# Kernel tuning notes

Hardware: AMD Instinct MI355X
Metric: run time of the kernel (lower is better)

The kernel has to match this reference:

```python
import jax, jax.numpy as jnp
import numpy as np

N_CHARS = 50257
CHAR = 512
HID = 1024
LENGTH = 2048


def setup_inputs() -> dict:
    key = jax.random.key(0)
    ks = jax.random.split(key, 8)
    s = 1.0 / np.sqrt(HID)
    sh = 1.0 / np.sqrt(HID)
    return {
        "inputs": jax.random.normal(ks[0], (HID,), jnp.float32),
        "embed": (jax.random.normal(ks[1], (N_CHARS, CHAR), jnp.float32) * 0.02),
        "W_ih": jax.random.uniform(ks[2], (4 * HID, CHAR), jnp.float32, -s, s),
        "W_hh": jax.random.uniform(ks[3], (4 * HID, HID), jnp.float32, -s, s),
        "b_ih": jax.random.uniform(ks[4], (4 * HID,), jnp.float32, -s, s),
        "b_hh": jax.random.uniform(ks[5], (4 * HID,), jnp.float32, -s, s),
        "W_head": jax.random.uniform(ks[6], (N_CHARS, HID), jnp.float32, -sh, sh),
        "b_head": jax.random.uniform(ks[7], (N_CHARS,), jnp.float32, -sh, sh),
        "length": LENGTH,
        "start": 5,
    }


def _lstm_cell(x, h, c, W_ih, W_hh, b_ih, b_hh):
    # PyTorch gate order: i, f, g, o
    gates = W_ih @ x + b_ih + W_hh @ h + b_hh  # [4H]
    i, f, g, o = jnp.split(gates, 4)
    i = jax.nn.sigmoid(i)
    f = jax.nn.sigmoid(f)
    g = jnp.tanh(g)
    o = jax.nn.sigmoid(o)
    c = f * c + i * g
    h = o * jnp.tanh(c)
    return h, c


def reference(inputs, embed, W_ih, W_hh, b_ih, b_hh, W_head, b_head, length, start):
    h0 = inputs                       # latent used as initial hidden state
    c0 = jnp.zeros_like(inputs)
    x0 = embed[start]                 # [CHAR]

    def step(carry, _):
        h, c, x = carry
        h, c = _lstm_cell(x, h, c, W_ih, W_hh, b_ih, b_hh)
        logits = W_head @ h + b_head  # [N_CHARS]
        char = jnp.argmax(logits)
        x = embed[char]
        return (h, c, x), (char, logits)

    _, (chars, logits) = jax.lax.scan(step, (h0, c0, x0), None, length=length)
    return chars, logits
```

## Files before the change

kernel.cpp:

```cpp
#include <hip/hip_runtime.h>
#include <stdint.h>
#include <math.h>

#define HID   1024
#define CHARD 512
#define NC    50257
#define TLEN  2048
#define NBS   1571
#define NBH   1571
#define SQ    4064.0f
#define INVSQ (1.0f/4064.0f)
#define QERR  (0.5f/4064.0f)
#define CANDR 256

typedef unsigned long long ull;
typedef unsigned char u8;
typedef float f32x4 __attribute__((ext_vector_type(4)));

__device__ __forceinline__ unsigned ford(float f) {
    unsigned b = __float_as_uint(f);
    return (b & 0x80000000u) ? ~b : (b | 0x80000000u);
}
__device__ __forceinline__ float unford(unsigned u) {
    return __uint_as_float((u & 0x80000000u) ? (u & 0x7FFFFFFFu) : ~u);
}
__device__ __forceinline__ ull packkv(float v, unsigned j) {
    return ((ull)ford(v) << 32) | (ull)(0xFFFFFFFFu - j);
}
__device__ __forceinline__ ull umaxu(ull a, ull b) { return a > b ? a : b; }
__device__ __forceinline__ ull shflx_ull(ull v, int m) {
    unsigned lo = (unsigned)v, hi = (unsigned)(v >> 32);
    lo = __shfl_xor(lo, m);
    hi = __shfl_xor(hi, m);
    return ((ull)hi << 32) | lo;
}

__global__ __launch_bounds__(256) void k_init(const float* __restrict__ inputs,
                                              float* __restrict__ hh,
                                              float* __restrict__ c)
{
    int tid = blockIdx.x * 256 + threadIdx.x;
    if (tid < HID) { hh[tid] = inputs[tid]; c[tid] = 0.f; }
}

__global__ __launch_bounds__(256) void k_quant(const float* __restrict__ W,
                                               u8* __restrict__ W8)
{
    size_t base = ((size_t)blockIdx.x * 256 + threadIdx.x) * 16;
    if (base >= (size_t)NC * HID) return;
    const float4* src = (const float4*)(W + base);
    uint out[4];
    #pragma unroll
    for (int g = 0; g < 4; ++g) {
        float4 w = src[g];
        int a0 = __float2int_rn(w.x * SQ) & 255;
        int a1 = __float2int_rn(w.y * SQ) & 255;
        int a2 = __float2int_rn(w.z * SQ) & 255;
        int a3 = __float2int_rn(w.w * SQ) & 255;
        out[g] = (uint)(a0 | (a1 << 8) | (a2 << 16) | (a3 << 24));
    }
    *(uint4*)(W8 + base) = make_uint4(out[0], out[1], out[2], out[3]);
}

__device__ __forceinline__ float exact_logit(const float4* hs4,
                                             const float* __restrict__ W_head,
                                             const float* __restrict__ b_head,
                                             int j, int lane)
{
    const float4* wr = (const float4*)(W_head + (size_t)j * HID);
    float a = 0.f;
    #pragma unroll
    for (int m = 0; m < 4; ++m) {
        float4 w = wr[m * 64 + lane], v = hs4[m * 64 + lane];
        a = fmaf(w.x, v.x, a); a = fmaf(w.y, v.y, a);
        a = fmaf(w.z, v.z, a); a = fmaf(w.w, v.w, a);
    }
    #pragma unroll
    for (int off = 32; off > 0; off >>= 1) a += __shfl_xor(a, off);
    return a + b_head[j];
}

__device__ __forceinline__ unsigned resolve_char(const float4* hs4,
                                                 const ull* __restrict__ blockmax,
                                                 const float* __restrict__ abuf,
                                                 const float* __restrict__ W_head,
                                                 const float* __restrict__ b_head,
                                                 float Sh, ull* red4, int tid)
{
    __shared__ int s_cnt;
    __shared__ int s_rows[CANDR];

    const int wave = tid >> 6;
    const int lane = tid & 63;

    ull pm = 0ull;
    for (int i = tid; i < NBS; i += 256) pm = umaxu(pm, blockmax[i]);
    #pragma unroll
    for (int off = 32; off > 0; off >>= 1) pm = umaxu(pm, shflx_ull(pm, off));
    if (lane == 0) red4[wave] = pm;
    if (tid == 0) s_cnt = 0;
    __syncthreads();
    pm = umaxu(umaxu(red4[0], red4[1]), umaxu(red4[2], red4[3]));
    const float mtil = unford((unsigned)(pm >> 32));
    const float E = QERR * Sh * 1.02f + 1e-4f;
    const float thresh = mtil - 2.0f * E;
    const ull pkth = ((ull)ford(thresh)) << 32;
    __syncthreads();

    for (int i = tid; i < NBS; i += 256) {
        if (blockmax[i] >= pkth) {
            const int jbase = i * 32;
            #pragma unroll
            for (int r = 0; r < 32; ++r) {
                const int j = jbase + r;
                if (j < NC && abuf[j] >= thresh) {
                    int p = atomicAdd(&s_cnt, 1);
                    if (p < CANDR) s_rows[p] = j;
                }
            }
        }
    }
    __syncthreads();
    const int ncr = s_cnt;

    ull best = 0ull;
    if (ncr <= CANDR) {
        for (int q = wave; q < ncr; q += 4) {
            const int j = s_rows[q];
            const float v = exact_logit(hs4, W_head, b_head, j, lane);
            best = umaxu(best, packkv(v, (unsigned)j));
        }
    } else {
        for (int i = wave; i < NBS; i += 4) {
            if (blockmax[i] >= pkth) {
                const int jbase = i * 32;
                for (int rr = 0; rr < 32; ++rr) {
                    const int j = jbase + rr;
                    if (j >= NC) break;
                    if (abuf[j] >= thresh) {
                        const float v = exact_logit(hs4, W_head, b_head, j, lane);
                        best = umaxu(best, packkv(v, (unsigned)j));
                    }
                }
            }
        }
    }
    __syncthreads();
    if (lane == 0) red4[wave] = best;
    __syncthreads();
    best = umaxu(umaxu(red4[0], red4[1]), umaxu(red4[2], red4[3]));
    unsigned idx = 0xFFFFFFFFu - (unsigned)(best & 0xFFFFFFFFull);
    return idx < NC ? idx : (NC - 1);
}

__global__ __launch_bounds__(256) void k_lstm(const float* __restrict__ W_ih,
                                              const float* __restrict__ W_hh,
                                              const float* __restrict__ b_ih,
                                              const float* __restrict__ b_hh,
                                              const float* __restrict__ embed,
                                              const float* __restrict__ W_head,
                                              const float* __restrict__ b_head,
                                              const ull* __restrict__ blockmax,
                                              const float* __restrict__ abuf,
                                              const float* __restrict__ h_in,
                                              float* __restrict__ h_out,
                                              float* __restrict__ c,
                                              float* __restrict__ chars_out,
                                              const int* __restrict__ startp,
                                              int t)
{
    __shared__ float4 xs4[CHARD / 4];
    __shared__ float4 hs4[HID / 4];
    __shared__ ull    red4[4];
    __shared__ float  sred[4];

    const int tid  = threadIdx.x;
    const int wave = tid >> 6;
    const int lane = tid & 63;

    float4 hv = ((const float4*)h_in)[tid];
    hs4[tid] = hv;
    float sa = fabsf(hv.x) + fabsf(hv.y) + fabsf(hv.z) + fabsf(hv.w);
    #pragma unroll
    for (int off = 32; off > 0; off >>= 1) sa += __shfl_xor(sa, off);
    if (lane == 0) sred[wave] = sa;
    __syncthreads();
    const float Sh = sred[0] + sred[1] + sred[2] + sred[3];

    unsigned idx;
    if (t == 0) {
        idx = (unsigned)startp[0];
    } else {
        idx = resolve_char(hs4, blockmax, abuf, W_head, b_head, Sh, red4, tid);
        if (blockIdx.x == 0 && tid == 0) chars_out[t - 1] = (float)idx;
    }

    const float4* ex = (const float4*)(embed + (size_t)idx * CHARD);
    if (tid < 128) xs4[tid] = ex[tid];
    __syncthreads();

    const int r = blockIdx.x * 4 + wave;

    float acc[4];
    #pragma unroll
    for (int q = 0; q < 4; ++q) {
        const float4* wi = (const float4*)(W_ih + (size_t)(q * HID + r) * CHARD);
        const float4* wh = (const float4*)(W_hh + (size_t)(q * HID + r) * HID);
        float a = 0.f;
        #pragma unroll
        for (int m = 0; m < 2; ++m) {
            float4 w = wi[m * 64 + lane], v = xs4[m * 64 + lane];
            a = fmaf(w.x, v.x, a); a = fmaf(w.y, v.y, a);
            a = fmaf(w.z, v.z, a); a = fmaf(w.w, v.w, a);
        }
        #pragma unroll
        for (int m = 0; m < 4; ++m) {
            float4 w = wh[m * 64 + lane], v = hs4[m * 64 + lane];
            a = fmaf(w.x, v.x, a); a = fmaf(w.y, v.y, a);
            a = fmaf(w.z, v.z, a); a = fmaf(w.w, v.w, a);
        }
        acc[q] = a;
    }
    #pragma unroll
    for (int q = 0; q < 4; ++q) {
        #pragma unroll
        for (int off = 32; off > 0; off >>= 1) acc[q] += __shfl_xor(acc[q], off);
    }

    if (lane == 0) {
        float zi = acc[0] + b_ih[r]           + b_hh[r];
        float zf = acc[1] + b_ih[HID + r]     + b_hh[HID + r];
        float zg = acc[2] + b_ih[2 * HID + r] + b_hh[2 * HID + r];
        float zo = acc[3] + b_ih[3 * HID + r] + b_hh[3 * HID + r];
        float ig = 1.f / (1.f + expf(-zi));
        float fg = 1.f / (1.f + expf(-zf));
        float gg = tanhf(zg);
        float og = 1.f / (1.f + expf(-zo));
        float cn = fg * c[r] + ig * gg;
        c[r] = cn;
        h_out[r] = og * tanhf(cn);
    }
}

__global__ __launch_bounds__(256) void k_screen(const u8* __restrict__ W8,
                                                const float* __restrict__ b_head,
                                                const float* __restrict__ h_in,
                                                float* __restrict__ abuf,
                                                ull* __restrict__ blockmax)
{
    __shared__ float4 hs4[HID / 4];
    __shared__ ull    wred[4];

    const int tid  = threadIdx.x;
    const int wave = tid >> 6;
    const int lane = tid & 63;

    hs4[tid] = ((const float4*)h_in)[tid];
    __syncthreads();

    const float4 h0 = hs4[lane * 4 + 0];
    const float4 h1 = hs4[lane * 4 + 1];
    const float4 h2 = hs4[lane * 4 + 2];
    const float4 h3 = hs4[lane * 4 + 3];

    const int base = blockIdx.x * 32 + wave * 8;
    ull pm = 0ull;
    #pragma unroll
    for (int rep = 0; rep < 8; ++rep) {
        const int j = base + rep;
        if (j < NC) {
            uint4 q = ((const uint4*)(W8 + (size_t)j * HID))[lane];
            float a = 0.f;
            a = fmaf((float)((int)(q.x << 24) >> 24), h0.x, a);
            a = fmaf((float)((int)(q.x << 16) >> 24), h0.y, a);
            a = fmaf((float)((int)(q.x <<  8) >> 24), h0.z, a);
            a = fmaf((float)((int)(q.x      ) >> 24), h0.w, a);
            a = fmaf((float)((int)(q.y << 24) >> 24), h1.x, a);
            a = fmaf((float)((int)(q.y << 16) >> 24), h1.y, a);
            a = fmaf((float)((int)(q.y <<  8) >> 24), h1.z, a);
            a = fmaf((float)((int)(q.y      ) >> 24), h1.w, a);
            a = fmaf((float)((int)(q.z << 24) >> 24), h2.x, a);
            a = fmaf((float)((int)(q.z << 16) >> 24), h2.y, a);
            a = fmaf((float)((int)(q.z <<  8) >> 24), h2.z, a);
            a = fmaf((float)((int)(q.z      ) >> 24), h2.w, a);
            a = fmaf((float)((int)(q.w << 24) >> 24), h3.x, a);
            a = fmaf((float)((int)(q.w << 16) >> 24), h3.y, a);
            a = fmaf((float)((int)(q.w <<  8) >> 24), h3.z, a);
            a = fmaf((float)((int)(q.w      ) >> 24), h3.w, a);
            #pragma unroll
            for (int off = 32; off > 0; off >>= 1) a += __shfl_xor(a, off);
            const float v = a * INVSQ + b_head[j];
            if (lane == 0) abuf[j] = v;
            pm = umaxu(pm, packkv(v, (unsigned)j));
        }
    }
    if (lane == 0) wred[wave] = pm;
    __syncthreads();
    if (tid == 0)
        blockmax[blockIdx.x] = umaxu(umaxu(wred[0], wred[1]), umaxu(wred[2], wred[3]));
}

__global__ __launch_bounds__(256) void k_finalc(const float* __restrict__ h_in,
                                                const ull* __restrict__ blockmax,
                                                const float* __restrict__ abuf,
                                                const float* __restrict__ W_head,
                                                const float* __restrict__ b_head,
                                                float* __restrict__ chars_out)
{
    __shared__ float4 hs4[HID / 4];
    __shared__ ull    red4[4];
    __shared__ float  sred[4];
    const int tid  = threadIdx.x;
    const int wave = tid >> 6;
    const int lane = tid & 63;

    float4 hv = ((const float4*)h_in)[tid];
    hs4[tid] = hv;
    float sa = fabsf(hv.x) + fabsf(hv.y) + fabsf(hv.z) + fabsf(hv.w);
    #pragma unroll
    for (int off = 32; off > 0; off >>= 1) sa += __shfl_xor(sa, off);
    if (lane == 0) sred[wave] = sa;
    __syncthreads();
    const float Sh = sred[0] + sred[1] + sred[2] + sred[3];
    unsigned idx = resolve_char(hs4, blockmax, abuf, W_head, b_head, Sh, red4, tid);
    if (tid == 0) chars_out[TLEN - 1] = (float)idx;
}

#define GJ 64
#define GT 128
#define GK 16
__global__ __launch_bounds__(256) void k_gemm(const float* __restrict__ W_head,
                                              const float* __restrict__ b_head,
                                              const float* __restrict__ hh,
                                              float* __restrict__ logits)
{
    __shared__ float Ws[GK][GJ + 4];
    __shared__ float Hs[GK][GT + 1];

    const int tid = threadIdx.x;
    const int j0 = blockIdx.x * GJ;
    const int t0 = blockIdx.y * GT;
    const int tj = tid & 15;
    const int tt = tid >> 4;

    const int wlj = tid >> 2;
    const int wlk = (tid & 3) * 4;
    const int hlt = tid >> 1;
    const int hlk = (tid & 1) * 8;
    const float* Wrow = W_head + (size_t)(j0 + wlj) * HID;
    const bool wvalid = (j0 + wlj) < NC;

    float acc[8][4];
    #pragma unroll
    for (int b = 0; b < 8; ++b)
        #pragma unroll
        for (int a = 0; a < 4; ++a) acc[b][a] = 0.f;

    for (int k0 = 0; k0 < HID; k0 += GK) {
        __syncthreads();
        float4 wv = wvalid ? *(const float4*)(Wrow + k0 + wlk) : make_float4(0, 0, 0, 0);
        Ws[wlk + 0][wlj] = wv.x; Ws[wlk + 1][wlj] = wv.y;
        Ws[wlk + 2][wlj] = wv.z; Ws[wlk + 3][wlj] = wv.w;
        const float* hp = hh + (size_t)(t0 + hlt + 1) * HID + k0 + hlk;
        float4 a0 = *(const float4*)hp;
        float4 a1 = *(const float4*)(hp + 4);
        Hs[hlk + 0][hlt] = a0.x; Hs[hlk + 1][hlt] = a0.y;
        Hs[hlk + 2][hlt] = a0.z; Hs[hlk + 3][hlt] = a0.w;
        Hs[hlk + 4][hlt] = a1.x; Hs[hlk + 5][hlt] = a1.y;
        Hs[hlk + 6][hlt] = a1.z; Hs[hlk + 7][hlt] = a1.w;
        __syncthreads();
        #pragma unroll
        for (int kk = 0; kk < GK; ++kk) {
            float4 w4 = *(const float4*)&Ws[kk][tj * 4];
            float hvv[8];
            #pragma unroll
            for (int b = 0; b < 8; ++b) hvv[b] = Hs[kk][tt + 16 * b];
            #pragma unroll
            for (int b = 0; b < 8; ++b) {
                acc[b][0] = fmaf(w4.x, hvv[b], acc[b][0]);
                acc[b][1] = fmaf(w4.y, hvv[b], acc[b][1]);
                acc[b][2] = fmaf(w4.z, hvv[b], acc[b][2]);
                acc[b][3] = fmaf(w4.w, hvv[b], acc[b][3]);
            }
        }
    }

    const int j = j0 + tj * 4;
    float b0 = (j + 0 < NC) ? b_head[j + 0] : 0.f;
    float b1 = (j + 1 < NC) ? b_head[j + 1] : 0.f;
    float b2 = (j + 2 < NC) ? b_head[j + 2] : 0.f;
    float b3 = (j + 3 < NC) ? b_head[j + 3] : 0.f;
    #pragma unroll
    for (int b = 0; b < 8; ++b) {
        const int t = t0 + tt + 16 * b;
        float* dst = logits + (size_t)t * NC + j;
        if (j + 3 < NC) {
            f32x4 o = { acc[b][0] + b0, acc[b][1] + b1,
                        acc[b][2] + b2, acc[b][3] + b3 };
            __builtin_nontemporal_store(o, (f32x4*)dst);
        } else {
            if (j + 0 < NC) dst[0] = acc[b][0] + b0;
            if (j + 1 < NC) dst[1] = acc[b][1] + b1;
            if (j + 2 < NC) dst[2] = acc[b][2] + b2;
        }
    }
}

__global__ __launch_bounds__(256) void k_init_fb(const float* __restrict__ inputs,
                                                 const int* __restrict__ startp,
                                                 float* __restrict__ h0,
                                                 float* __restrict__ c,
                                                 ull* __restrict__ blockmax)
{
    int tid = blockIdx.x * 256 + threadIdx.x;
    if (tid < NBH) blockmax[tid] = (tid == 0) ? packkv(3.0e38f, (unsigned)startp[0]) : 0ull;
    if (tid < HID) { h0[tid] = inputs[tid]; c[tid] = 0.f; }
}

__global__ __launch_bounds__(256) void k_lstm_fb(const float* __restrict__ W_ih,
                                                 const float* __restrict__ W_hh,
                                                 const float* __restrict__ b_ih,
                                                 const float* __restrict__ b_hh,
                                                 const float* __restrict__ embed,
                                                 const ull* __restrict__ blockmax,
                                                 const float* __restrict__ h_in,
                                                 float* __restrict__ h_out,
                                                 float* __restrict__ c,
                                                 float* __restrict__ chars_out,
                                                 int t)
{
    __shared__ float4 xs4[CHARD / 4];
    __shared__ float4 hs4[HID / 4];
    __shared__ ull    red[256];
    const int tid = threadIdx.x;
    ull pm = 0ull;
    for (int i = tid; i < NBH; i += 256) pm = umaxu(pm, blockmax[i]);
    red[tid] = pm;
    __syncthreads();
    for (int s = 128; s > 0; s >>= 1) {
        if (tid < s) red[tid] = umaxu(red[tid], red[tid + s]);
        __syncthreads();
    }
    const unsigned idx = 0xFFFFFFFFu - (unsigned)(red[0] & 0xFFFFFFFFull);
    if (t > 0 && blockIdx.x == 0 && tid == 0) chars_out[t - 1] = (float)idx;
    const float4* ex = (const float4*)(embed + (size_t)idx * CHARD);
    if (tid < 128) xs4[tid] = ex[tid];
    hs4[tid] = ((const float4*)h_in)[tid];
    __syncthreads();
    const int wave = tid >> 6, lane = tid & 63;
    const int r = blockIdx.x * 4 + wave;
    float acc[4];
    #pragma unroll
    for (int q = 0; q < 4; ++q) {
        const float4* wi = (const float4*)(W_ih + (size_t)(q * HID + r) * CHARD);
        const float4* wh = (const float4*)(W_hh + (size_t)(q * HID + r) * HID);
        float a = 0.f;
        #pragma unroll
        for (int m = 0; m < 2; ++m) {
            float4 w = wi[m * 64 + lane], v = xs4[m * 64 + lane];
            a = fmaf(w.x, v.x, a); a = fmaf(w.y, v.y, a);
            a = fmaf(w.z, v.z, a); a = fmaf(w.w, v.w, a);
        }
        #pragma unroll
        for (int m = 0; m < 4; ++m) {
            float4 w = wh[m * 64 + lane], v = hs4[m * 64 + lane];
            a = fmaf(w.x, v.x, a); a = fmaf(w.y, v.y, a);
            a = fmaf(w.z, v.z, a); a = fmaf(w.w, v.w, a);
        }
        acc[q] = a;
    }
    #pragma unroll
    for (int q = 0; q < 4; ++q)
        #pragma unroll
        for (int off = 32; off > 0; off >>= 1) acc[q] += __shfl_xor(acc[q], off);
    if (lane == 0) {
        float zi = acc[0] + b_ih[r]           + b_hh[r];
        float zf = acc[1] + b_ih[HID + r]     + b_hh[HID + r];
        float zg = acc[2] + b_ih[2 * HID + r] + b_hh[2 * HID + r];
        float zo = acc[3] + b_ih[3 * HID + r] + b_hh[3 * HID + r];
        float ig = 1.f / (1.f + expf(-zi));
        float fg = 1.f / (1.f + expf(-zf));
        float gg = tanhf(zg);
        float og = 1.f / (1.f + expf(-zo));
        float cn = fg * c[r] + ig * gg;
        c[r] = cn;
        h_out[r] = og * tanhf(cn);
    }
}

__global__ __launch_bounds__(256) void k_head_fb(const float* __restrict__ W_head,
                                                 const float* __restrict__ b_head,
                                                 const float* __restrict__ h_in,
                                                 float* __restrict__ logits,
                                                 ull* __restrict__ blockmax)
{
    __shared__ float4 hs4[HID / 4];
    __shared__ ull    wmax[4];
    const int tid = threadIdx.x;
    hs4[tid] = ((const float4*)h_in)[tid];
    __syncthreads();
    const int wave = tid >> 6, lane = tid & 63;
    const int base = blockIdx.x * 32 + wave * 8;
    ull pm = 0ull;
    #pragma unroll
    for (int rep = 0; rep < 8; ++rep) {
        const int j = base + rep;
        if (j < NC) {
            const float4* w = (const float4*)(W_head + (size_t)j * HID);
            float a = 0.f;
            #pragma unroll
            for (int m = 0; m < 4; ++m) {
                float4 ww = w[m * 64 + lane], v = hs4[m * 64 + lane];
                a = fmaf(ww.x, v.x, a); a = fmaf(ww.y, v.y, a);
                a = fmaf(ww.z, v.z, a); a = fmaf(ww.w, v.w, a);
            }
            #pragma unroll
            for (int off = 32; off > 0; off >>= 1) a += __shfl_xor(a, off);
            const float v = a + b_head[j];
            if (lane == 0) __builtin_nontemporal_store(v, &logits[j]);
            pm = umaxu(pm, packkv(v, (unsigned)j));
        }
    }
    if (lane == 0) wmax[wave] = pm;
    __syncthreads();
    if (tid == 0)
        blockmax[blockIdx.x] = umaxu(umaxu(wmax[0], wmax[1]), umaxu(wmax[2], wmax[3]));
}

__global__ __launch_bounds__(256) void k_final_fb(const ull* __restrict__ blockmax,
                                                  float* __restrict__ chars_out)
{
    __shared__ ull red[256];
    const int tid = threadIdx.x;
    ull pm = 0ull;
    for (int i = tid; i < NBH; i += 256) pm = umaxu(pm, blockmax[i]);
    red[tid] = pm;
    __syncthreads();
    for (int s = 128; s > 0; s >>= 1) {
        if (tid < s) red[tid] = umaxu(red[tid], red[tid + s]);
        __syncthreads();
    }
    if (tid == 0)
        chars_out[TLEN - 1] = (float)(0xFFFFFFFFu - (unsigned)(red[0] & 0xFFFFFFFFull));
}

extern "C" void kernel_launch(void* const* d_in, const int* in_sizes, int n_in,
                              void* d_out, int out_size, void* d_ws, size_t ws_size,
                              hipStream_t stream)
{
    const float* inputs = (const float*)d_in[0];
    const float* embed  = (const float*)d_in[1];
    const float* W_ih   = (const float*)d_in[2];
    const float* W_hh   = (const float*)d_in[3];
    const float* b_ih   = (const float*)d_in[4];
    const float* b_hh   = (const float*)d_in[5];
    const float* W_head = (const float*)d_in[6];
    const float* b_head = (const float*)d_in[7];
    const int*   startp = (const int*)d_in[9];

    float* out        = (float*)d_out;
    float* chars_out  = out;
    float* logits_out = out + TLEN;

    char* ws = (char*)d_ws;
    const size_t off_hh = 0;
    const size_t off_c  = off_hh + (size_t)(TLEN + 1) * HID * 4;
    const size_t off_ab = off_c + (size_t)HID * 4;
    const size_t off_bm = (off_ab + (size_t)NC * 4 + 7) & ~(size_t)7;
    const size_t off_w8 = (off_bm + (size_t)NBS * 8 + 15) & ~(size_t)15;
    const size_t need   = off_w8 + (size_t)NC * HID;

    if (ws_size >= need) {
        float* hh   = (float*)(ws + off_hh);
        float* c    = (float*)(ws + off_c);
        float* abuf = (float*)(ws + off_ab);
        ull*   bm   = (ull*)(ws + off_bm);
        u8*    W8   = (u8*)(ws + off_w8);

        hipLaunchKernelGGL(k_init, dim3(4), dim3(256), 0, stream, inputs, hh, c);
        hipLaunchKernelGGL(k_quant, dim3((NC * HID / 16 + 255) / 256), dim3(256), 0, stream,
                           W_head, W8);

        for (int t = 0; t < TLEN; ++t) {
            hipLaunchKernelGGL(k_lstm, dim3(256), dim3(256), 0, stream,
                               W_ih, W_hh, b_ih, b_hh, embed, W_head, b_head,
                               bm, abuf, hh + (size_t)t * HID, hh + (size_t)(t + 1) * HID,
                               c, chars_out, startp, t);
            hipLaunchKernelGGL(k_screen, dim3(NBS), dim3(256), 0, stream,
                               W8, b_head, hh + (size_t)(t + 1) * HID, abuf, bm);
        }
        hipLaunchKernelGGL(k_finalc, dim3(1), dim3(256), 0, stream,
                           hh + (size_t)TLEN * HID, bm, abuf, W_head, b_head, chars_out);
        hipLaunchKernelGGL(k_gemm, dim3((NC + GJ - 1) / GJ, TLEN / GT), dim3(256), 0, stream,
                           W_head, b_head, hh, logits_out);
    } else {
        float* h0 = (float*)(ws);
        float* h1 = (float*)(ws + 4096);
        float* c  = (float*)(ws + 8192);
        ull* blockmax = (ull*)(ws + 12288);
        hipLaunchKernelGGL(k_init_fb, dim3(7), dim3(256), 0, stream,
                           inputs, startp, h0, c, blockmax);
        for (int t = 0; t < TLEN; ++t) {
            const float* hin = (t & 1) ? h1 : h0;
            float*       hout = (t & 1) ? h0 : h1;
            hipLaunchKernelGGL(k_lstm_fb, dim3(256), dim3(256), 0, stream,
                               W_ih, W_hh, b_ih, b_hh, embed, blockmax,
                               hin, hout, c, chars_out, t);
            hipLaunchKernelGGL(k_head_fb, dim3(NBH), dim3(256), 0, stream,
                               W_head, b_head, hout,
                               logits_out + (size_t)t * NC, blockmax);
        }
        hipLaunchKernelGGL(k_final_fb, dim3(1), dim3(256), 0, stream, blockmax, chars_out);
    }
}
```

Before: 54.27 ms.

## Fuse per-step LSTM and screen kernels into one persistent kernel with grid barriers

Replaces the 4096 per-step kernel launches (LSTM cell plus int8 head screening) with a single persistent 256-block kernel that loops over all timesteps, using a custom flag-based grid barrier between phases. Each block caches its W_ih/W_hh rows in shared memory and keeps the cell state in a register. The head screening is re-partitioned into 1024 groups of 50 rows, one per wave. This removes launch overhead and repeated weight reloads. In exchange it relies on all 256 blocks being co-resident, and the spin barrier carries a deadlock/timeout risk and its own synchronisation cost.

```diff
diff --git a/kernel.cpp b/kernel.cpp
--- a/kernel.cpp
+++ b/kernel.cpp
@@ -6,12 +6,15 @@
 #define CHARD 512
 #define NC    50257
 #define TLEN  2048
-#define NBS   1571
+#define NBLK  256
+#define NGRP2 1024
+#define GR    50
 #define NBH   1571
 #define SQ    4064.0f
 #define INVSQ (1.0f/4064.0f)
 #define QERR  (0.5f/4064.0f)
 #define CANDR 256
+#define FLAGSTRIDE 16
 
 typedef unsigned long long ull;
 typedef unsigned char u8;
@@ -35,12 +38,48 @@
     return ((ull)hi << 32) | lo;
 }
 
+__device__ __forceinline__ void gridbar(unsigned* flags, unsigned* gen,
+                                        unsigned k, int b, int tid)
+{
+    __syncthreads();
+    if (b == 0) {
+        if (tid == 0) {
+            __threadfence();
+            __hip_atomic_store(&flags[0], k, __ATOMIC_RELAXED, __HIP_MEMORY_SCOPE_AGENT);
+        }
+        unsigned v; int guard = 0;
+        do {
+            v = __hip_atomic_load(&flags[tid * FLAGSTRIDE], __ATOMIC_RELAXED,
+                                  __HIP_MEMORY_SCOPE_AGENT);
+        } while (v < k && ++guard < (1 << 27));
+        __syncthreads();
+        if (tid == 0)
+            __hip_atomic_store(gen, k, __ATOMIC_RELAXED, __HIP_MEMORY_SCOPE_AGENT);
+    } else {
+        if (tid == 0) {
+            __threadfence();
+            __hip_atomic_store(&flags[b * FLAGSTRIDE], k, __ATOMIC_RELAXED,
+                               __HIP_MEMORY_SCOPE_AGENT);
+            unsigned v; int guard = 0;
+            do {
+                __builtin_amdgcn_s_sleep(1);
+                v = __hip_atomic_load(gen, __ATOMIC_RELAXED, __HIP_MEMORY_SCOPE_AGENT);
+            } while (v < k && ++guard < (1 << 27));
+        }
+        __syncthreads();
+    }
+    if (tid == 0) __threadfence();
+    __syncthreads();
+}
+
 __global__ __launch_bounds__(256) void k_init(const float* __restrict__ inputs,
                                               float* __restrict__ hh,
-                                              float* __restrict__ c)
-{
-    int tid = blockIdx.x * 256 + threadIdx.x;
-    if (tid < HID) { hh[tid] = inputs[tid]; c[tid] = 0.f; }
+                                              float* __restrict__ c,
+                                              unsigned* __restrict__ flagarea)
+{
+    int g = blockIdx.x * 256 + threadIdx.x;
+    if (g < HID) { hh[g] = inputs[g]; c[g] = 0.f; }
+    for (int i = g; i < NBLK * FLAGSTRIDE + 16; i += 2048) flagarea[i] = 0u;
 }
 
 __global__ __launch_bounds__(256) void k_quant(const float* __restrict__ W,
@@ -81,7 +120,7 @@
 }
 
 __device__ __forceinline__ unsigned resolve_char(const float4* hs4,
-                                                 const ull* __restrict__ blockmax,
+                                                 const ull* __restrict__ bm,
                                                  const float* __restrict__ abuf,
                                                  const float* __restrict__ W_head,
                                                  const float* __restrict__ b_head,
@@ -94,7 +133,9 @@
     const int lane = tid & 63;
 
     ull pm = 0ull;
-    for (int i = tid; i < NBS; i += 256) pm = umaxu(pm, blockmax[i]);
+    #pragma unroll
+    for (int rep = 0; rep < NGRP2 / 256; ++rep)
+        pm = umaxu(pm, bm[tid + rep * 256]);
     #pragma unroll
     for (int off = 32; off > 0; off >>= 1) pm = umaxu(pm, shflx_ull(pm, off));
     if (lane == 0) red4[wave] = pm;
@@ -107,13 +148,14 @@
     const ull pkth = ((ull)ford(thresh)) << 32;
     __syncthreads();
 
-    for (int i = tid; i < NBS; i += 256) {
-        if (blockmax[i] >= pkth) {
-            const int jbase = i * 32;
-            #pragma unroll
-            for (int r = 0; r < 32; ++r) {
-                const int j = jbase + r;
-                if (j < NC && abuf[j] >= thresh) {
+    #pragma unroll
+    for (int rep = 0; rep < NGRP2 / 256; ++rep) {
+        const int i = tid + rep * 256;
+        if (bm[i] >= pkth) {
+            const int jb = i * GR;
+            const int je = jb + GR < NC ? jb + GR : NC;
+            for (int j = jb; j < je; ++j) {
+                if (abuf[j] >= thresh) {
                     int p = atomicAdd(&s_cnt, 1);
                     if (p < CANDR) s_rows[p] = j;
                 }
@@ -127,20 +169,18 @@
     if (ncr <= CANDR) {
         for (int q = wave; q < ncr; q += 4) {
             const int j = s_rows[q];
-            const float v = exact_logit(hs4, W_head, b_head, j, lane);
-            best = umaxu(best, packkv(v, (unsigned)j));
+            best = umaxu(best, packkv(exact_logit(hs4, W_head, b_head, j, lane),
+                                      (unsigned)j));
         }
     } else {
-        for (int i = wave; i < NBS; i += 4) {
-            if (blockmax[i] >= pkth) {
-                const int jbase = i * 32;
-                for (int rr = 0; rr < 32; ++rr) {
-                    const int j = jbase + rr;
-                    if (j >= NC) break;
-                    if (abuf[j] >= thresh) {
-                        const float v = exact_logit(hs4, W_head, b_head, j, lane);
-                        best = umaxu(best, packkv(v, (unsigned)j));
-                    }
+        for (int i = wave; i < NGRP2; i += 4) {
+            if (bm[i] >= pkth) {
+                const int jb = i * GR;
+                const int je = jb + GR < NC ? jb + GR : NC;
+                for (int j = jb; j < je; ++j) {
+                    if (abuf[j] >= thresh)
+                        best = umaxu(best, packkv(exact_logit(hs4, W_head, b_head, j, lane),
+                                                  (unsigned)j));
                 }
             }
         }
@@ -153,177 +193,157 @@
     return idx < NC ? idx : (NC - 1);
 }
 
-__global__ __launch_bounds__(256) void k_lstm(const float* __restrict__ W_ih,
-                                              const float* __restrict__ W_hh,
-                                              const float* __restrict__ b_ih,
-                                              const float* __restrict__ b_hh,
-                                              const float* __restrict__ embed,
-                                              const float* __restrict__ W_head,
-                                              const float* __restrict__ b_head,
-                                              const ull* __restrict__ blockmax,
-                                              const float* __restrict__ abuf,
-                                              const float* __restrict__ h_in,
-                                              float* __restrict__ h_out,
-                                              float* __restrict__ c,
-                                              float* __restrict__ chars_out,
-                                              const int* __restrict__ startp,
-                                              int t)
-{
+__global__ __launch_bounds__(256) void k_persist(
+    const float* __restrict__ W_ih, const float* __restrict__ W_hh,
+    const float* __restrict__ b_ih, const float* __restrict__ b_hh,
+    const float* __restrict__ embed,
+    const float* __restrict__ W_head, const float* __restrict__ b_head,
+    const u8* __restrict__ W8,
+    float* __restrict__ hh, float* __restrict__ abuf, ull* __restrict__ bm,
+    float* __restrict__ chars_out, const int* __restrict__ startp,
+    unsigned* flags, unsigned* gen)
+{
+    __shared__ float4 wiL[4][4][128];
+    __shared__ float4 whL[4][4][256];
     __shared__ float4 xs4[CHARD / 4];
     __shared__ float4 hs4[HID / 4];
     __shared__ ull    red4[4];
     __shared__ float  sred[4];
 
+    const int b    = blockIdx.x;
     const int tid  = threadIdx.x;
     const int wave = tid >> 6;
     const int lane = tid & 63;
-
-    float4 hv = ((const float4*)h_in)[tid];
-    hs4[tid] = hv;
-    float sa = fabsf(hv.x) + fabsf(hv.y) + fabsf(hv.z) + fabsf(hv.w);
-    #pragma unroll
-    for (int off = 32; off > 0; off >>= 1) sa += __shfl_xor(sa, off);
-    if (lane == 0) sred[wave] = sa;
-    __syncthreads();
-    const float Sh = sred[0] + sred[1] + sred[2] + sred[3];
-
-    unsigned idx;
-    if (t == 0) {
-        idx = (unsigned)startp[0];
-    } else {
-        idx = resolve_char(hs4, blockmax, abuf, W_head, b_head, Sh, red4, tid);
-        if (blockIdx.x == 0 && tid == 0) chars_out[t - 1] = (float)idx;
-    }
-
-    const float4* ex = (const float4*)(embed + (size_t)idx * CHARD);
-    if (tid < 128) xs4[tid] = ex[tid];
-    __syncthreads();
-
-    const int r = blockIdx.x * 4 + wave;
-
-    float acc[4];
-    #pragma unroll
+    const int r    = b * 4 + wave;
+
     for (int q = 0; q < 4; ++q) {
         const float4* wi = (const float4*)(W_ih + (size_t)(q * HID + r) * CHARD);
+        for (int m = lane; m < 128; m += 64) wiL[wave][q][m] = wi[m];
         const float4* wh = (const float4*)(W_hh + (size_t)(q * HID + r) * HID);
-        float a = 0.f;
-        #pragma unroll
-        for (int m = 0; m < 2; ++m) {
-            float4 w = wi[m * 64 + lane], v = xs4[m * 64 + lane];
-            a = fmaf(w.x, v.x, a); a = fmaf(w.y, v.y, a);
-            a = fmaf(w.z, v.z, a); a = fmaf(w.w, v.w, a);
-        }
-        #pragma unroll
-        for (int m = 0; m < 4; ++m) {
-            float4 w = wh[m * 64 + lane], v = hs4[m * 64 + lane];
-            a = fmaf(w.x, v.x, a); a = fmaf(w.y, v.y, a);
-            a = fmaf(w.z, v.z, a); a = fmaf(w.w, v.w, a);
-        }
-        acc[q] = a;
-    }
-    #pragma unroll
-    for (int q = 0; q < 4; ++q) {
-        #pragma unroll
-        for (int off = 32; off > 0; off >>= 1) acc[q] += __shfl_xor(acc[q], off);
-    }
-
-    if (lane == 0) {
-        float zi = acc[0] + b_ih[r]           + b_hh[r];
-        float zf = acc[1] + b_ih[HID + r]     + b_hh[HID + r];
-        float zg = acc[2] + b_ih[2 * HID + r] + b_hh[2 * HID + r];
-        float zo = acc[3] + b_ih[3 * HID + r] + b_hh[3 * HID + r];
-        float ig = 1.f / (1.f + expf(-zi));
-        float fg = 1.f / (1.f + expf(-zf));
-        float gg = tanhf(zg);
-        float og = 1.f / (1.f + expf(-zo));
-        float cn = fg * c[r] + ig * gg;
-        c[r] = cn;
-        h_out[r] = og * tanhf(cn);
-    }
-}
-
-__global__ __launch_bounds__(256) void k_screen(const u8* __restrict__ W8,
-                                                const float* __restrict__ b_head,
-                                                const float* __restrict__ h_in,
-                                                float* __restrict__ abuf,
-                                                ull* __restrict__ blockmax)
-{
-    __shared__ float4 hs4[HID / 4];
-    __shared__ ull    wred[4];
-
-    const int tid  = threadIdx.x;
-    const int wave = tid >> 6;
-    const int lane = tid & 63;
-
-    hs4[tid] = ((const float4*)h_in)[tid];
-    __syncthreads();
-
-    const float4 h0 = hs4[lane * 4 + 0];
-    const float4 h1 = hs4[lane * 4 + 1];
-    const float4 h2 = hs4[lane * 4 + 2];
-    const float4 h3 = hs4[lane * 4 + 3];
-
-    const int base = blockIdx.x * 32 + wave * 8;
-    ull pm = 0ull;
-    #pragma unroll
-    for (int rep = 0; rep < 8; ++rep) {
-        const int j = base + rep;
-        if (j < NC) {
-            uint4 q = ((const uint4*)(W8 + (size_t)j * HID))[lane];
+        for (int m = lane; m < 256; m += 64) whL[wave][q][m] = wh[m];
+    }
+    float bsum[4];
+    #pragma unroll
+    for (int q = 0; q < 4; ++q) bsum[q] = b_ih[q * HID + r] + b_hh[q * HID + r];
+    float creg = 0.f;
+    __syncthreads();
+
+    unsigned bk = 0;
+
+    for (int t = 0; t < TLEN; ++t) {
+        float4 hv = ((const float4*)(hh + (size_t)t * HID))[tid];
+        hs4[tid] = hv;
+        float sa = fabsf(hv.x) + fabsf(hv.y) + fabsf(hv.z) + fabsf(hv.w);
+        #pragma unroll
+        for (int off = 32; off > 0; off >>= 1) sa += __shfl_xor(sa, off);
+        if (lane == 0) sred[wave] = sa;
+        __syncthreads();
+        const float Sh = sred[0] + sred[1] + sred[2] + sred[3];
+
+        unsigned idx;
+        if (t == 0) {
+            idx = (unsigned)startp[0];
+        } else {
+            idx = resolve_char(hs4, bm, abuf, W_head, b_head, Sh, red4, tid);
+            if (b == 0 && tid == 0) chars_out[t - 1] = (float)idx;
+        }
+        if (tid < 128) xs4[tid] = ((const float4*)(embed + (size_t)idx * CHARD))[tid];
+        __syncthreads();
+
+        float acc[4];
+        #pragma unroll
+        for (int q = 0; q < 4; ++q) {
             float a = 0.f;
-            a = fmaf((float)((int)(q.x << 24) >> 24), h0.x, a);
-            a = fmaf((float)((int)(q.x << 16) >> 24), h0.y, a);
-            a = fmaf((float)((int)(q.x <<  8) >> 24), h0.z, a);
-            a = fmaf((float)((int)(q.x      ) >> 24), h0.w, a);
-            a = fmaf((float)((int)(q.y << 24) >> 24), h1.x, a);
-            a = fmaf((float)((int)(q.y << 16) >> 24), h1.y, a);
-            a = fmaf((float)((int)(q.y <<  8) >> 24), h1.z, a);
-            a = fmaf((float)((int)(q.y      ) >> 24), h1.w, a);
-            a = fmaf((float)((int)(q.z << 24) >> 24), h2.x, a);
-            a = fmaf((float)((int)(q.z << 16) >> 24), h2.y, a);
-            a = fmaf((float)((int)(q.z <<  8) >> 24), h2.z, a);
-            a = fmaf((float)((int)(q.z      ) >> 24), h2.w, a);
-            a = fmaf((float)((int)(q.w << 24) >> 24), h3.x, a);
-            a = fmaf((float)((int)(q.w << 16) >> 24), h3.y, a);
-            a = fmaf((float)((int)(q.w <<  8) >> 24), h3.z, a);
-            a = fmaf((float)((int)(q.w      ) >> 24), h3.w, a);
             #pragma unroll
-            for (int off = 32; off > 0; off >>= 1) a += __shfl_xor(a, off);
-            const float v = a * INVSQ + b_head[j];
-            if (lane == 0) abuf[j] = v;
-            pm = umaxu(pm, packkv(v, (unsigned)j));
-        }
-    }
-    if (lane == 0) wred[wave] = pm;
-    __syncthreads();
-    if (tid == 0)
-        blockmax[blockIdx.x] = umaxu(umaxu(wred[0], wred[1]), umaxu(wred[2], wred[3]));
-}
-
-__global__ __launch_bounds__(256) void k_finalc(const float* __restrict__ h_in,
-                                                const ull* __restrict__ blockmax,
-                                                const float* __restrict__ abuf,
-                                                const float* __restrict__ W_head,
-                                                const float* __restrict__ b_head,
-                                                float* __restrict__ chars_out)
-{
-    __shared__ float4 hs4[HID / 4];
-    __shared__ ull    red4[4];
-    __shared__ float  sred[4];
-    const int tid  = threadIdx.x;
-    const int wave = tid >> 6;
-    const int lane = tid & 63;
-
-    float4 hv = ((const float4*)h_in)[tid];
-    hs4[tid] = hv;
-    float sa = fabsf(hv.x) + fabsf(hv.y) + fabsf(hv.z) + fabsf(hv.w);
-    #pragma unroll
-    for (int off = 32; off > 0; off >>= 1) sa += __shfl_xor(sa, off);
-    if (lane == 0) sred[wave] = sa;
-    __syncthreads();
-    const float Sh = sred[0] + sred[1] + sred[2] + sred[3];
-    unsigned idx = resolve_char(hs4, blockmax, abuf, W_head, b_head, Sh, red4, tid);
-    if (tid == 0) chars_out[TLEN - 1] = (float)idx;
+            for (int m = 0; m < 2; ++m) {
+                float4 w = wiL[wave][q][m * 64 + lane], v = xs4[m * 64 + lane];
+                a = fmaf(w.x, v.x, a); a = fmaf(w.y, v.y, a);
+                a = fmaf(w.z, v.z, a); a = fmaf(w.w, v.w, a);
+            }
+            #pragma unroll
+            for (int m = 0; m < 4; ++m) {
+                float4 w = whL[wave][q][m * 64 + lane], v = hs4[m * 64 + lane];
+                a = fmaf(w.x, v.x, a); a = fmaf(w.y, v.y, a);
+                a = fmaf(w.z, v.z, a); a = fmaf(w.w, v.w, a);
+            }
+            acc[q] = a;
+        }
+        #pragma unroll
+        for (int q = 0; q < 4; ++q) {
+            #pragma unroll
+            for (int off = 32; off > 0; off >>= 1) acc[q] += __shfl_xor(acc[q], off);
+        }
+        if (lane == 0) {
+            float zi = acc[0] + bsum[0];
+            float zf = acc[1] + bsum[1];
+            float zg = acc[2] + bsum[2];
+            float zo = acc[3] + bsum[3];
+            float ig = 1.f / (1.f + expf(-zi));
+            float fg = 1.f / (1.f + expf(-zf));
+            float gg = tanhf(zg);
+            float og = 1.f / (1.f + expf(-zo));
+            creg = fg * creg + ig * gg;
+            hh[(size_t)(t + 1) * HID + r] = og * tanhf(creg);
+        }
+
+        gridbar(flags, gen, ++bk, b, tid);
+
+        float4 hn = ((const float4*)(hh + (size_t)(t + 1) * HID))[tid];
+        hs4[tid] = hn;
+        __syncthreads();
+        const float4 h0 = hs4[lane * 4 + 0];
+        const float4 h1 = hs4[lane * 4 + 1];
+        const float4 h2 = hs4[lane * 4 + 2];
+        const float4 h3 = hs4[lane * 4 + 3];
+
+        const int jb = r * GR;
+        ull pmw = 0ull;
+        #pragma unroll 2
+        for (int rr = 0; rr < GR; ++rr) {
+            const int j = jb + rr;
+            if (j < NC) {
+                uint4 qv = ((const uint4*)(W8 + (size_t)j * HID))[lane];
+                float a = 0.f;
+                a = fmaf((float)((int)(qv.x << 24) >> 24), h0.x, a);
+                a = fmaf((float)((int)(qv.x << 16) >> 24), h0.y, a);
+                a = fmaf((float)((int)(qv.x <<  8) >> 24), h0.z, a);
+                a = fmaf((float)((int)(qv.x      ) >> 24), h0.w, a);
+                a = fmaf((float)((int)(qv.y << 24) >> 24), h1.x, a);
+                a = fmaf((float)((int)(qv.y << 16) >> 24), h1.y, a);
+                a = fmaf((float)((int)(qv.y <<  8) >> 24), h1.z, a);
+                a = fmaf((float)((int)(qv.y      ) >> 24), h1.w, a);
+                a = fmaf((float)((int)(qv.z << 24) >> 24), h2.x, a);
+                a = fmaf((float)((int)(qv.z << 16) >> 24), h2.y, a);
+                a = fmaf((float)((int)(qv.z <<  8) >> 24), h2.z, a);
+                a = fmaf((float)((int)(qv.z      ) >> 24), h2.w, a);
+                a = fmaf((float)((int)(qv.w << 24) >> 24), h3.x, a);
+                a = fmaf((float)((int)(qv.w << 16) >> 24), h3.y, a);
+                a = fmaf((float)((int)(qv.w <<  8) >> 24), h3.z, a);
+                a = fmaf((float)((int)(qv.w      ) >> 24), h3.w, a);
+                #pragma unroll
+                for (int off = 32; off > 0; off >>= 1) a += __shfl_xor(a, off);
+                const float v = a * INVSQ + b_head[j];
+                if (lane == 0) abuf[j] = v;
+                pmw = umaxu(pmw, packkv(v, (unsigned)j));
+            }
+        }
+        if (lane == 0) bm[r] = pmw;
+
+        gridbar(flags, gen, ++bk, b, tid);
+    }
+
+    if (b == 0) {
+        float4 hv = ((const float4*)(hh + (size_t)TLEN * HID))[tid];
+        hs4[tid] = hv;
+        float sa = fabsf(hv.x) + fabsf(hv.y) + fabsf(hv.z) + fabsf(hv.w);
+        #pragma unroll
+        for (int off = 32; off > 0; off >>= 1) sa += __shfl_xor(sa, off);
+        if (lane == 0) sred[wave] = sa;
+        __syncthreads();
+        const float Sh = sred[0] + sred[1] + sred[2] + sred[3];
+        unsigned idx = resolve_char(hs4, bm, abuf, W_head, b_head, Sh, red4, tid);
+        if (tid == 0) chars_out[TLEN - 1] = (float)idx;
+    }
 }
 
 #define GJ 64
@@ -352,9 +372,9 @@
 
     float acc[8][4];
     #pragma unroll
-    for (int b = 0; b < 8; ++b)
-        #pragma unroll
-        for (int a = 0; a < 4; ++a) acc[b][a] = 0.f;
+    for (int bb = 0; bb < 8; ++bb)
+        #pragma unroll
+        for (int a = 0; a < 4; ++a) acc[bb][a] = 0.f;
 
     for (int k0 = 0; k0 < HID; k0 += GK) {
         __syncthreads();
@@ -374,13 +394,13 @@
             float4 w4 = *(const float4*)&Ws[kk][tj * 4];
             float hvv[8];
             #pragma unroll
-            for (int b = 0; b < 8; ++b) hvv[b] = Hs[kk][tt + 16 * b];
+            for (int bb = 0; bb < 8; ++bb) hvv[bb] = Hs[kk][tt + 16 * bb];
             #pragma unroll
-            for (int b = 0; b < 8; ++b) {
-                acc[b][0] = fmaf(w4.x, hvv[b], acc[b][0]);
-                acc[b][1] = fmaf(w4.y, hvv[b], acc[b][1]);
-                acc[b][2] = fmaf(w4.z, hvv[b], acc[b][2]);
-                acc[b][3] = fmaf(w4.w, hvv[b], acc[b][3]);
+            for (int bb = 0; bb < 8; ++bb) {
+                acc[bb][0] = fmaf(w4.x, hvv[bb], acc[bb][0]);
+                acc[bb][1] = fmaf(w4.y, hvv[bb], acc[bb][1]);
+                acc[bb][2] = fmaf(w4.z, hvv[bb], acc[bb][2]);
+                acc[bb][3] = fmaf(w4.w, hvv[bb], acc[bb][3]);
             }
         }
     }
@@ -391,17 +411,17 @@
     float b2 = (j + 2 < NC) ? b_head[j + 2] : 0.f;
     float b3 = (j + 3 < NC) ? b_head[j + 3] : 0.f;
     #pragma unroll
-    for (int b = 0; b < 8; ++b) {
-        const int t = t0 + tt + 16 * b;
+    for (int bb = 0; bb < 8; ++bb) {
+        const int t = t0 + tt + 16 * bb;
         float* dst = logits + (size_t)t * NC + j;
         if (j + 3 < NC) {
-            f32x4 o = { acc[b][0] + b0, acc[b][1] + b1,
-                        acc[b][2] + b2, acc[b][3] + b3 };
+            f32x4 o = { acc[bb][0] + b0, acc[bb][1] + b1,
+                        acc[bb][2] + b2, acc[bb][3] + b3 };
             __builtin_nontemporal_store(o, (f32x4*)dst);
         } else {
-            if (j + 0 < NC) dst[0] = acc[b][0] + b0;
-            if (j + 1 < NC) dst[1] = acc[b][1] + b1;
-            if (j + 2 < NC) dst[2] = acc[b][2] + b2;
+            if (j + 0 < NC) dst[0] = acc[bb][0] + b0;
+            if (j + 1 < NC) dst[1] = acc[bb][1] + b1;
+            if (j + 2 < NC) dst[2] = acc[bb][2] + b2;
         }
     }
 }
@@ -563,36 +583,32 @@
     float* logits_out = out + TLEN;
 
     char* ws = (char*)d_ws;
-    const size_t off_hh = 0;
-    const size_t off_c  = off_hh + (size_t)(TLEN + 1) * HID * 4;
-    const size_t off_ab = off_c + (size_t)HID * 4;
-    const size_t off_bm = (off_ab + (size_t)NC * 4 + 7) & ~(size_t)7;
-    const size_t off_w8 = (off_bm + (size_t)NBS * 8 + 15) & ~(size_t)15;
-    const size_t need   = off_w8 + (size_t)NC * HID;
+    const size_t off_hh    = 0;
+    const size_t off_c     = off_hh + (size_t)(TLEN + 1) * HID * 4;
+    const size_t off_ab    = off_c + (size_t)HID * 4;
+    const size_t off_bm    = (off_ab + (size_t)NC * 4 + 15) & ~(size_t)15;
+    const size_t off_flags = (off_bm + (size_t)NGRP2 * 8 + 63) & ~(size_t)63;
+    const size_t off_w8    = (off_flags + (size_t)(NBLK * FLAGSTRIDE + 16) * 4 + 15)
+                             & ~(size_t)15;
+    const size_t need      = off_w8 + (size_t)NC * HID;
 
     if (ws_size >= need) {
-        float* hh   = (float*)(ws + off_hh);
-        float* c    = (float*)(ws + off_c);
-        float* abuf = (float*)(ws + off_ab);
-        ull*   bm   = (ull*)(ws + off_bm);
-        u8*    W8   = (u8*)(ws + off_w8);
-
-        hipLaunchKernelGGL(k_init, dim3(4), dim3(256), 0, stream, inputs, hh, c);
-        hipLaunchKernelGGL(k_quant, dim3((NC * HID / 16 + 255) / 256), dim3(256), 0, stream,
-                           W_head, W8);
-
-        for (int t = 0; t < TLEN; ++t) {
-            hipLaunchKernelGGL(k_lstm, dim3(256), dim3(256), 0, stream,
-                               W_ih, W_hh, b_ih, b_hh, embed, W_head, b_head,
-                               bm, abuf, hh + (size_t)t * HID, hh + (size_t)(t + 1) * HID,
-                               c, chars_out, startp, t);
-            hipLaunchKernelGGL(k_screen, dim3(NBS), dim3(256), 0, stream,
-                               W8, b_head, hh + (size_t)(t + 1) * HID, abuf, bm);
-        }
-        hipLaunchKernelGGL(k_finalc, dim3(1), dim3(256), 0, stream,
-                           hh + (size_t)TLEN * HID, bm, abuf, W_head, b_head, chars_out);
-        hipLaunchKernelGGL(k_gemm, dim3((NC + GJ - 1) / GJ, TLEN / GT), dim3(256), 0, stream,
-                           W_head, b_head, hh, logits_out);
+        float*    hh    = (float*)(ws + off_hh);
+        float*    c     = (float*)(ws + off_c);
+        float*    abuf  = (float*)(ws + off_ab);
+        ull*      bm    = (ull*)(ws + off_bm);
+        unsigned* flags = (unsigned*)(ws + off_flags);
+        unsigned* gen   = flags + NBLK * FLAGSTRIDE;
+        u8*       W8    = (u8*)(ws + off_w8);
+
+        hipLaunchKernelGGL(k_init, dim3(8), dim3(256), 0, stream, inputs, hh, c, flags);
+        hipLaunchKernelGGL(k_quant, dim3((NC * HID / 16 + 255) / 256), dim3(256), 0,
+                           stream, W_head, W8);
+        hipLaunchKernelGGL(k_persist, dim3(NBLK), dim3(256), 0, stream,
+                           W_ih, W_hh, b_ih, b_hh, embed, W_head, b_head, W8,
+                           hh, abuf, bm, chars_out, startp, flags, gen);
+        hipLaunchKernelGGL(k_gemm, dim3((NC + GJ - 1) / GJ, TLEN / GT), dim3(256), 0,
+                           stream, W_head, b_head, hh, logits_out);
     } else {
         float* h0 = (float*)(ws);
         float* h1 = (float*)(ws + 4096);
```

After: 136.6 ms. 2.52x slower.
